# Kernel optimization log

Hardware: AMD Instinct MI355X
Metric: run time of the kernel (lower is better)

The kernel has to match this reference:

```python
import jax, jax.numpy as jnp
import numpy as np

V = 5023      # CoMA mesh vertices
K = 8         # avg neighbors per vertex
E = V * K     # edges
B = 64        # batch
C_IN = 3      # xyz
C_HID = 64    # conv width (layer_info)
M = 9         # kernel_size: number of weight matrices
LATENT = 128


def fsc_conv(x, src, dst, aw, u, c, W, b):
    """Feature-steered graph conv (translation invariant: v = -u).
    x: [B,V,C]; edge e: (i=src[e], j=dst[e]) with adjacency weight aw[e].
    y_i = b + sum_j a_ij * sum_m softmax_m(u_m.(x_i-x_j)+c_m) * (x_j @ W_m)
    """
    Bx, Vx, C = x.shape
    D = W.shape[2]
    xi = x[:, src]                                  # [B,E,C]
    xj = x[:, dst]                                  # [B,E,C]
    logits = jnp.einsum('bec,cm->bem', xi - xj, u) + c   # [B,E,M]
    att = jax.nn.softmax(logits, axis=-1) * aw[None, :, None]
    y = jnp.zeros((Bx, Vx, D), x.dtype)
    for m in range(W.shape[0]):                     # small fixed loop over M
        agg = jnp.zeros((Bx, Vx, C), x.dtype).at[:, src].add(att[:, :, m:m + 1] * xj)
        y = y + agg @ W[m]
    return y + b


def setup_inputs() -> dict:
    key = jax.random.key(0)
    ks = jax.random.split(key, 16)
    x = jax.random.normal(ks[0], (B, V, C_IN), jnp.float32)
    # mesh-like adjacency: each vertex i has K random neighbors, weight 1/K
    src = jnp.repeat(jnp.arange(V, dtype=jnp.int32), K)
    dst = jax.random.randint(ks[1], (E,), 0, V, dtype=jnp.int32)
    aw = jnp.full((E,), 1.0 / K, jnp.float32)
    g = lambda k, shp, fan: jax.random.normal(k, shp, jnp.float32) * np.float32(np.sqrt(2.0 / fan))
    # encoder conv params
    u_e = g(ks[2], (C_IN, M), C_IN + M)
    c_e = jnp.zeros((M,), jnp.float32)
    W_e = g(ks[3], (M, C_IN, C_HID), C_IN + C_HID)
    b_e = jnp.zeros((C_HID,), jnp.float32)
    # encoder latent dense: [V*C_HID, LATENT]
    W_enc = g(ks[4], (V * C_HID, LATENT), V * C_HID)
    b_enc = jnp.zeros((LATENT,), jnp.float32)
    # decoder latent dense: [LATENT, C_HID*V]
    W_dec = g(ks[5], (LATENT, C_HID * V), LATENT)
    b_dec = jnp.zeros((C_HID * V,), jnp.float32)
    # decoder conv params
    u_d = g(ks[6], (C_HID, M), C_HID + M)
    c_d = jnp.zeros((M,), jnp.float32)
    W_d = g(ks[7], (M, C_HID, C_IN), C_HID + C_IN)
    b_d = jnp.zeros((C_IN,), jnp.float32)
    return {'x': x, 'aw': aw, 'u_e': u_e, 'c_e': c_e, 'W_e': W_e, 'b_e': b_e,
            'W_enc': W_enc, 'b_enc': b_enc, 'W_dec': W_dec, 'b_dec': b_dec,
            'u_d': u_d, 'c_d': c_d, 'W_d': W_d, 'b_d': b_d,
            'src': src, 'dst': dst}


def reference(x, aw, u_e, c_e, W_e, b_e, W_enc, b_enc, W_dec, b_dec,
              u_d, c_d, W_d, b_d, src, dst):
    # Encoder: feature-steered conv -> relu -> flatten -> dense to latent
    h = jax.nn.relu(fsc_conv(x, src, dst, aw, u_e, c_e, W_e, b_e))   # [B,V,C_HID]
    z = h.reshape(h.shape[0], -1) @ W_enc + b_enc                    # [B,LATENT]
    # Decoder: dense -> reshape [B,V,C_HID] -> feature-steered conv -> relu
    d = (z @ W_dec + b_dec).reshape(z.shape[0], V, -1)               # [B,V,C_HID]
    out = jax.nn.relu(fsc_conv(d, src, dst, aw, u_d, c_d, W_d, b_d)) # [B,V,3]
    return out
```

## Files before the change

### kernel.cpp

```cpp
#include <hip/hip_runtime.h>

#define VN 5023
#define KN 8
#define BN 64
#define CIN 3
#define CH 64
#define MN 9
#define LAT 128
#define KTOT (VN*CH)
#define NBV (BN*VN)
#define KC 256
#define NCHUNK 1256
#define RED_G 8
#define RED_J 157
#define NXCD 8

__global__ __launch_bounds__(256, 4) void k_conv1(
    const float* __restrict__ x, const float* __restrict__ aw,
    const int* __restrict__ dst,
    const float* __restrict__ u_e, const float* __restrict__ c_e,
    const float* __restrict__ W_e, const float* __restrict__ b_e,
    float* __restrict__ h)
{
  int t = blockIdx.x*256 + threadIdx.x;
  if (t >= NBV) return;
  int b = t / VN, v = t - b*VN;
  const float* xb = x + (size_t)b*VN*CIN;
  float xi0 = xb[v*3+0], xi1 = xb[v*3+1], xi2 = xb[v*3+2];
  float Ti[MN];
#pragma unroll
  for (int m=0;m<MN;m++)
    Ti[m] = xi0*u_e[m] + xi1*u_e[MN+m] + xi2*u_e[2*MN+m] + c_e[m];
  float agg[27];
#pragma unroll
  for (int i=0;i<27;i++) agg[i]=0.f;
  for (int k=0;k<KN;k++){
    int e = v*KN+k;
    int j = dst[e];
    float awe = aw[e];
    float xj0 = xb[j*3+0], xj1 = xb[j*3+1], xj2 = xb[j*3+2];
    float lg[MN];
#pragma unroll
    for (int m=0;m<MN;m++)
      lg[m] = Ti[m] - (xj0*u_e[m]+xj1*u_e[MN+m]+xj2*u_e[2*MN+m]);
    float mx = lg[0];
#pragma unroll
    for (int m=1;m<MN;m++) mx = fmaxf(mx, lg[m]);
    float ex[MN], s=0.f;
#pragma unroll
    for (int m=0;m<MN;m++){ ex[m] = __expf(lg[m]-mx); s += ex[m]; }
    float r = awe / s;
#pragma unroll
    for (int m=0;m<MN;m++){
      float a = ex[m]*r;
      agg[m*3+0] += a*xj0; agg[m*3+1] += a*xj1; agg[m*3+2] += a*xj2;
    }
  }
  float* hr = h + (size_t)t*CH;
  for (int cc=0; cc<4; cc++){
    float y[16];
#pragma unroll
    for (int c=0;c<16;c++) y[c] = b_e[cc*16+c];
#pragma unroll
    for (int mc=0; mc<27; mc++){
      float a = agg[mc];
#pragma unroll
      for (int c=0;c<16;c++) y[c] += a * W_e[mc*CH + cc*16 + c];
    }
#pragma unroll
    for (int c=0;c<16;c+=4){
      float4 o = make_float4(fmaxf(y[c],0.f),fmaxf(y[c+1],0.f),
                             fmaxf(y[c+2],0.f),fmaxf(y[c+3],0.f));
      *(float4*)(hr + cc*16 + c) = o;
    }
  }
}

__global__ __launch_bounds__(256, 4) void k_enc(
    const float* __restrict__ h, const float* __restrict__ We,
    float* __restrict__ partial)
{
  __shared__ float wlds[2][32*128];
  __shared__ float hlds[2][32][68];
  int t = threadIdx.x;
  int blk = blockIdx.x;
  int lq = t & 15;
  int bq = t >> 4;
  float acc[8][4];
#pragma unroll
  for (int i=0;i<8;i++)
#pragma unroll
    for (int j=0;j<4;j++) acc[i][j]=0.f;
  int kbase0 = blk*KC;
  int ldb = t & 63;
  int seg = t >> 6;
  int nt0 = (blk == NCHUNK-1) ? 6 : 8;

  float4 wreg0, wreg1, wreg2, wreg3, hreg0, hreg1;
  {
    const float* wsrc = We + (size_t)kbase0*LAT;
    wreg0 = *(const float4*)(wsrc + 0*1024 + t*4);
    wreg1 = *(const float4*)(wsrc + 1*1024 + t*4);
    wreg2 = *(const float4*)(wsrc + 2*1024 + t*4);
    wreg3 = *(const float4*)(wsrc + 3*1024 + t*4);
    const float* hsrc = h + (size_t)ldb*KTOT + kbase0 + seg*8;
    hreg0 = *(const float4*)(hsrc);
    hreg1 = *(const float4*)(hsrc + 4);
    *(float4*)(&wlds[0][0*1024 + t*4]) = wreg0;
    *(float4*)(&wlds[0][1*1024 + t*4]) = wreg1;
    *(float4*)(&wlds[0][2*1024 + t*4]) = wreg2;
    *(float4*)(&wlds[0][3*1024 + t*4]) = wreg3;
    hlds[0][seg*8+0][ldb]=hreg0.x; hlds[0][seg*8+1][ldb]=hreg0.y;
    hlds[0][seg*8+2][ldb]=hreg0.z; hlds[0][seg*8+3][ldb]=hreg0.w;
    hlds[0][seg*8+4][ldb]=hreg1.x; hlds[0][seg*8+5][ldb]=hreg1.y;
    hlds[0][seg*8+6][ldb]=hreg1.z; hlds[0][seg*8+7][ldb]=hreg1.w;
  }
  __syncthreads();

  int cur = 0;
  for (int t0=0; t0<nt0; t0++){
    bool pf = (t0+1 < nt0);
    if (pf){
      int kbase = kbase0 + (t0+1)*32;
      const float* wsrc = We + (size_t)kbase*LAT;
      wreg0 = *(const float4*)(wsrc + 0*1024 + t*4);
      wreg1 = *(const float4*)(wsrc + 1*1024 + t*4);
      wreg2 = *(const float4*)(wsrc + 2*1024 + t*4);
      wreg3 = *(const float4*)(wsrc + 3*1024 + t*4);
      const float* hsrc = h + (size_t)ldb*KTOT + kbase + seg*8;
      hreg0 = *(const float4*)(hsrc);
      hreg1 = *(const float4*)(hsrc + 4);
    }
    __builtin_amdgcn_sched_barrier(0);
#pragma unroll 4
    for (int kk=0; kk<32; kk++){
      const float* wr = &wlds[cur][kk*128 + lq*8];
      float4 w0 = *(const float4*)wr;
      float4 w1 = *(const float4*)(wr+4);
      float4 z  = *(const float4*)(&hlds[cur][kk][bq*4]);
      float wv[8] = {w0.x,w0.y,w0.z,w0.w,w1.x,w1.y,w1.z,w1.w};
      float zv[4] = {z.x,z.y,z.z,z.w};
#pragma unroll
      for (int li=0;li<8;li++)
#pragma unroll
        for (int bi=0;bi<4;bi++) acc[li][bi] += wv[li]*zv[bi];
    }
    if (pf){
      int nb = cur^1;
      *(float4*)(&wlds[nb][0*1024 + t*4]) = wreg0;
      *(float4*)(&wlds[nb][1*1024 + t*4]) = wreg1;
      *(float4*)(&wlds[nb][2*1024 + t*4]) = wreg2;
      *(float4*)(&wlds[nb][3*1024 + t*4]) = wreg3;
      hlds[nb][seg*8+0][ldb]=hreg0.x; hlds[nb][seg*8+1][ldb]=hreg0.y;
      hlds[nb][seg*8+2][ldb]=hreg0.z; hlds[nb][seg*8+3][ldb]=hreg0.w;
      hlds[nb][seg*8+4][ldb]=hreg1.x; hlds[nb][seg*8+5][ldb]=hreg1.y;
      hlds[nb][seg*8+6][ldb]=hreg1.z; hlds[nb][seg*8+7][ldb]=hreg1.w;
    }
    __syncthreads();
    cur ^= 1;
  }
  float* pp = partial + (size_t)blk*(BN*LAT);
#pragma unroll
  for (int bi=0;bi<4;bi++){
    int b = bq*4+bi;
    float4 o0 = make_float4(acc[0][bi],acc[1][bi],acc[2][bi],acc[3][bi]);
    float4 o1 = make_float4(acc[4][bi],acc[5][bi],acc[6][bi],acc[7][bi]);
    *(float4*)(pp + b*LAT + lq*8)   = o0;
    *(float4*)(pp + b*LAT + lq*8+4) = o1;
  }
}

__global__ __launch_bounds__(256) void k_red1(
    const float* __restrict__ partial, float* __restrict__ partial2)
{
  int idx = blockIdx.x*256 + threadIdx.x;
  int g = blockIdx.y;
  float s = 0.f;
  for (int j=0;j<RED_J;j++)
    s += partial[(size_t)(g + RED_G*j)*(BN*LAT) + idx];
  partial2[(size_t)g*(BN*LAT) + idx] = s;
}

__global__ __launch_bounds__(256) void k_red2(
    const float* __restrict__ partial2, const float* __restrict__ b_enc,
    float* __restrict__ zT)
{
  int idx = blockIdx.x*256 + threadIdx.x;
  float s = 0.f;
#pragma unroll
  for (int g=0; g<RED_G; g++) s += partial2[(size_t)g*(BN*LAT) + idx];
  int b = idx >> 7, l = idx & 127;
  zT[l*BN + b] = s + b_enc[l];
}

__global__ __launch_bounds__(512, 4) void k_dec(
    const float* __restrict__ zT, const float* __restrict__ Wd,
    const float* __restrict__ b_dec, float* __restrict__ d)
{
  int t = threadIdx.x;
  int lane = t & 63;
  int wv = __builtin_amdgcn_readfirstlane(t >> 6);
  int vc = blockIdx.x*256 + lane*4;
  int vs = vc < (KTOT-4) ? vc : (KTOT-4);
  const float* wp = Wd + vs;
  const float* zrow = zT + wv*8;
  float acc[4][8];
#pragma unroll
  for (int i=0;i<4;i++)
#pragma unroll
    for (int j=0;j<8;j++) acc[i][j]=0.f;

  float4 wA[4], wB[4];
#pragma unroll
  for (int u=0;u<4;u++) wA[u] = *(const float4*)(wp + (size_t)u*KTOT);

  for (int l0=0; l0<LAT; l0+=8){
#pragma unroll
    for (int u=0;u<4;u++) wB[u] = *(const float4*)(wp + (size_t)(l0+4+u)*KTOT);
    __builtin_amdgcn_sched_barrier(0);
#pragma unroll
    for (int u=0;u<4;u++){
      int l = l0+u;
      float zv[8];
#pragma unroll
      for (int j=0;j<8;j++) zv[j] = zrow[l*BN + j];
      float wvv[4] = {wA[u].x,wA[u].y,wA[u].z,wA[u].w};
#pragma unroll
      for (int i=0;i<4;i++)
#pragma unroll
        for (int j=0;j<8;j++) acc[i][j] += wvv[i]*zv[j];
    }
    if (l0+8 < LAT){
#pragma unroll
      for (int u=0;u<4;u++) wA[u] = *(const float4*)(wp + (size_t)(l0+8+u)*KTOT);
    }
    __builtin_amdgcn_sched_barrier(0);
#pragma unroll
    for (int u=0;u<4;u++){
      int l = l0+4+u;
      float zv[8];
#pragma unroll
      for (int j=0;j<8;j++) zv[j] = zrow[l*BN + j];
      float wvv[4] = {wB[u].x,wB[u].y,wB[u].z,wB[u].w};
#pragma unroll
      for (int i=0;i<4;i++)
#pragma unroll
        for (int j=0;j<8;j++) acc[i][j] += wvv[i]*zv[j];
    }
  }
  if (vc < KTOT){
    float4 bd = *(const float4*)(b_dec + vc);
#pragma unroll
    for (int j=0;j<8;j++){
      int b = wv*8 + j;
      float4 o = make_float4(acc[0][j]+bd.x, acc[1][j]+bd.y,
                             acc[2][j]+bd.z, acc[3][j]+bd.w);
      *(float4*)(d + (size_t)b*KTOT + vc) = o;
    }
  }
}

__global__ __launch_bounds__(256, 4) void k_tg(
    const float* __restrict__ d, const float* __restrict__ u_d,
    const float* __restrict__ W_d, float* __restrict__ TG)
{
  int t = blockIdx.x*256 + threadIdx.x;
  if (t >= NBV) return;
  const float* drow = d + (size_t)t*CH;
  float T[MN], G[27];
#pragma unroll
  for (int m=0;m<MN;m++) T[m]=0.f;
#pragma unroll
  for (int i=0;i<27;i++) G[i]=0.f;
  for (int c0=0;c0<CH;c0+=4){
    float4 dv = *(const float4*)(drow+c0);
    float dvv[4] = {dv.x,dv.y,dv.z,dv.w};
#pragma unroll
    for (int j=0;j<4;j++){
      int c = c0+j;
      float xv = dvv[j];
#pragma unroll
      for (int m=0;m<MN;m++) T[m] += xv*u_d[c*MN+m];
#pragma unroll
      for (int m=0;m<MN;m++){
        G[m*3+0] += xv*W_d[(m*CH+c)*3+0];
        G[m*3+1] += xv*W_d[(m*CH+c)*3+1];
        G[m*3+2] += xv*W_d[(m*CH+c)*3+2];
      }
    }
  }
  float* tg = TG + (size_t)t*36;
  float rr[36] = {T[0],T[1],T[2],T[3],T[4],T[5],T[6],T[7],T[8],
                  G[0],G[1],G[2],G[3],G[4],G[5],G[6],G[7],G[8],
                  G[9],G[10],G[11],G[12],G[13],G[14],G[15],G[16],G[17],
                  G[18],G[19],G[20],G[21],G[22],G[23],G[24],G[25],G[26]};
#pragma unroll
  for (int i=0;i<36;i+=4)
    *(float4*)(tg+i) = make_float4(rr[i],rr[i+1],rr[i+2],rr[i+3]);
}

__global__ __launch_bounds__(256, 4) void k_att(
    const float* __restrict__ TG, const float* __restrict__ aw,
    const int* __restrict__ dst, const float* __restrict__ c_d,
    const float* __restrict__ b_d, float* __restrict__ out)
{
  int wg = blockIdx.x;
  int wgid = (wg & 7)*157 + (wg >> 3);
  int t = wgid*256 + threadIdx.x;
  if (t >= NBV) return;
  int b = t / VN, v = t - b*VN;
  const float* TGb = TG + (size_t)b*VN*36;
  int e0 = v*KN;
  int4 j01 = *(const int4*)(dst + e0);
  int4 j23 = *(const int4*)(dst + e0 + 4);
  int jj[8] = {j01.x,j01.y,j01.z,j01.w, j23.x,j23.y,j23.z,j23.w};
  float4 a01 = *(const float4*)(aw + e0);
  float4 a23 = *(const float4*)(aw + e0 + 4);
  float awv[8] = {a01.x,a01.y,a01.z,a01.w, a23.x,a23.y,a23.z,a23.w};
  float Ti[MN];
#pragma unroll
  for (int m=0;m<MN;m++) Ti[m] = TGb[(size_t)v*36+m] + c_d[m];
  float y0=0.f, y1=0.f, y2=0.f;
  float4 q[9];
  {
    const float* Rp = TGb + (size_t)jj[0]*36;
#pragma unroll
    for (int i=0;i<9;i++) q[i] = *(const float4*)(Rp + i*4);
  }
#pragma unroll
  for (int k=0;k<KN;k++){
    float4 p[9];
    if (k+1 < KN){
      const float* Rp = TGb + (size_t)jj[k+1]*36;
#pragma unroll
      for (int i=0;i<9;i++) p[i] = *(const float4*)(Rp + i*4);
    }
    float rr[36] = {q[0].x,q[0].y,q[0].z,q[0].w, q[1].x,q[1].y,q[1].z,q[1].w,
                    q[2].x,q[2].y,q[2].z,q[2].w, q[3].x,q[3].y,q[3].z,q[3].w,
                    q[4].x,q[4].y,q[4].z,q[4].w, q[5].x,q[5].y,q[5].z,q[5].w,
                    q[6].x,q[6].y,q[6].z,q[6].w, q[7].x,q[7].y,q[7].z,q[7].w,
                    q[8].x,q[8].y,q[8].z,q[8].w};
    float lg[MN];
#pragma unroll
    for (int m=0;m<MN;m++) lg[m] = Ti[m] - rr[m];
    float mx = lg[0];
#pragma unroll
    for (int m=1;m<MN;m++) mx = fmaxf(mx, lg[m]);
    float ex[MN], s=0.f;
#pragma unroll
    for (int m=0;m<MN;m++){ ex[m] = __expf(lg[m]-mx); s += ex[m]; }
    float sc = awv[k] / s;
#pragma unroll
    for (int m=0;m<MN;m++){
      float a = ex[m]*sc;
      y0 += a*rr[9+m*3+0]; y1 += a*rr[9+m*3+1]; y2 += a*rr[9+m*3+2];
    }
    if (k+1 < KN){
#pragma unroll
      for (int i=0;i<9;i++) q[i] = p[i];
    }
  }
  float* o = out + (size_t)t*3;
  o[0]=fmaxf(y0+b_d[0],0.f); o[1]=fmaxf(y1+b_d[1],0.f); o[2]=fmaxf(y2+b_d[2],0.f);
}

extern "C" void kernel_launch(void* const* d_in, const int* in_sizes, int n_in,
                              void* d_out, int out_size, void* d_ws, size_t ws_size,
                              hipStream_t stream) {
  const float* x     = (const float*)d_in[0];
  const float* aw    = (const float*)d_in[1];
  const float* u_e   = (const float*)d_in[2];
  const float* c_e   = (const float*)d_in[3];
  const float* W_e   = (const float*)d_in[4];
  const float* b_e   = (const float*)d_in[5];
  const float* W_enc = (const float*)d_in[6];
  const float* b_enc = (const float*)d_in[7];
  const float* W_dec = (const float*)d_in[8];
  const float* b_dec = (const float*)d_in[9];
  const float* u_d   = (const float*)d_in[10];
  const float* c_d   = (const float*)d_in[11];
  const float* W_d   = (const float*)d_in[12];
  const float* b_d   = (const float*)d_in[13];
  const int*   dst   = (const int*)d_in[15];
  float* out = (float*)d_out;

  char* ws = (char*)d_ws;
  float* hbuf = (float*)ws;
  size_t off1 = (size_t)NBV*CH*sizeof(float);
  float* partial = (float*)(ws + off1);
  float* TGbuf   = (float*)(ws + off1);
  size_t offz = off1 + (size_t)NCHUNK*(BN*LAT)*sizeof(float);
  float* zT       = (float*)(ws + offz);
  float* partial2 = (float*)(ws + offz + (size_t)(BN*LAT)*sizeof(float));

  int grid_bv = (NBV + 255)/256;

  k_conv1<<<grid_bv,256,0,stream>>>(x, aw, dst, u_e, c_e, W_e, b_e, hbuf);
  k_enc<<<NCHUNK,256,0,stream>>>(hbuf, W_enc, partial);
  dim3 gr1(32, RED_G);
  k_red1<<<gr1,256,0,stream>>>(partial, partial2);
  k_red2<<<32,256,0,stream>>>(partial2, b_enc, zT);
  int grid_dec = (KTOT + 255)/256;
  k_dec<<<grid_dec,512,0,stream>>>(zT, W_dec, b_dec, hbuf);
  k_tg<<<grid_bv,256,0,stream>>>(hbuf, u_d, W_d, TGbuf);
  k_att<<<grid_bv,256,0,stream>>>(TGbuf, aw, dst, c_d, b_d, out);
}
```

Baseline: 347.6 us.

## Use direct global-to-LDS loads in encoder GEMM, larger K chunks, batched conv1 gathers

```diff
diff --git a/kernel.cpp b/kernel.cpp
--- a/kernel.cpp
+++ b/kernel.cpp
@@ -9,9 +9,9 @@
 #define LAT 128
 #define KTOT (VN*CH)
 #define NBV (BN*VN)
-#define KC 256
-#define NCHUNK 1256
-#define RED_G 8
+#define KC 512
+#define NCHUNK 628
+#define RED_G 4
 #define RED_J 157
 #define NXCD 8
 
@@ -26,6 +26,20 @@
   if (t >= NBV) return;
   int b = t / VN, v = t - b*VN;
   const float* xb = x + (size_t)b*VN*CIN;
+  int e0 = v*KN;
+  int4 j01 = *(const int4*)(dst + e0);
+  int4 j23 = *(const int4*)(dst + e0 + 4);
+  int jj[8] = {j01.x,j01.y,j01.z,j01.w, j23.x,j23.y,j23.z,j23.w};
+  float4 a01 = *(const float4*)(aw + e0);
+  float4 a23 = *(const float4*)(aw + e0 + 4);
+  float awv[8] = {a01.x,a01.y,a01.z,a01.w, a23.x,a23.y,a23.z,a23.w};
+  float xj0[8], xj1[8], xj2[8];
+#pragma unroll
+  for (int k=0;k<KN;k++){
+    const float* xr = xb + (size_t)jj[k]*3;
+    xj0[k]=xr[0]; xj1[k]=xr[1]; xj2[k]=xr[2];
+  }
+  __builtin_amdgcn_sched_barrier(0);
   float xi0 = xb[v*3+0], xi1 = xb[v*3+1], xi2 = xb[v*3+2];
   float Ti[MN];
 #pragma unroll
@@ -34,26 +48,23 @@
   float agg[27];
 #pragma unroll
   for (int i=0;i<27;i++) agg[i]=0.f;
+#pragma unroll
   for (int k=0;k<KN;k++){
-    int e = v*KN+k;
-    int j = dst[e];
-    float awe = aw[e];
-    float xj0 = xb[j*3+0], xj1 = xb[j*3+1], xj2 = xb[j*3+2];
     float lg[MN];
 #pragma unroll
     for (int m=0;m<MN;m++)
-      lg[m] = Ti[m] - (xj0*u_e[m]+xj1*u_e[MN+m]+xj2*u_e[2*MN+m]);
+      lg[m] = Ti[m] - (xj0[k]*u_e[m]+xj1[k]*u_e[MN+m]+xj2[k]*u_e[2*MN+m]);
     float mx = lg[0];
 #pragma unroll
     for (int m=1;m<MN;m++) mx = fmaxf(mx, lg[m]);
     float ex[MN], s=0.f;
 #pragma unroll
     for (int m=0;m<MN;m++){ ex[m] = __expf(lg[m]-mx); s += ex[m]; }
-    float r = awe / s;
+    float r = awv[k] / s;
 #pragma unroll
     for (int m=0;m<MN;m++){
       float a = ex[m]*r;
-      agg[m*3+0] += a*xj0; agg[m*3+1] += a*xj1; agg[m*3+2] += a*xj2;
+      agg[m*3+0] += a*xj0[k]; agg[m*3+1] += a*xj1[k]; agg[m*3+2] += a*xj2[k];
     }
   }
   float* hr = h + (size_t)t*CH;
@@ -94,22 +105,19 @@
   int kbase0 = blk*KC;
   int ldb = t & 63;
   int seg = t >> 6;
-  int nt0 = (blk == NCHUNK-1) ? 6 : 8;
-
-  float4 wreg0, wreg1, wreg2, wreg3, hreg0, hreg1;
+  int nt0 = (blk == NCHUNK-1) ? 14 : 16;
+
   {
     const float* wsrc = We + (size_t)kbase0*LAT;
-    wreg0 = *(const float4*)(wsrc + 0*1024 + t*4);
-    wreg1 = *(const float4*)(wsrc + 1*1024 + t*4);
-    wreg2 = *(const float4*)(wsrc + 2*1024 + t*4);
-    wreg3 = *(const float4*)(wsrc + 3*1024 + t*4);
+#pragma unroll
+    for (int q=0;q<4;q++)
+      __builtin_amdgcn_global_load_lds(
+        (const __attribute__((address_space(1))) void*)(wsrc + (q*256+t)*4),
+        (__attribute__((address_space(3))) void*)(&wlds[0][(q*256+t)*4]),
+        16, 0, 0);
     const float* hsrc = h + (size_t)ldb*KTOT + kbase0 + seg*8;
-    hreg0 = *(const float4*)(hsrc);
-    hreg1 = *(const float4*)(hsrc + 4);
-    *(float4*)(&wlds[0][0*1024 + t*4]) = wreg0;
-    *(float4*)(&wlds[0][1*1024 + t*4]) = wreg1;
-    *(float4*)(&wlds[0][2*1024 + t*4]) = wreg2;
-    *(float4*)(&wlds[0][3*1024 + t*4]) = wreg3;
+    float4 hreg0 = *(const float4*)(hsrc);
+    float4 hreg1 = *(const float4*)(hsrc + 4);
     hlds[0][seg*8+0][ldb]=hreg0.x; hlds[0][seg*8+1][ldb]=hreg0.y;
     hlds[0][seg*8+2][ldb]=hreg0.z; hlds[0][seg*8+3][ldb]=hreg0.w;
     hlds[0][seg*8+4][ldb]=hreg1.x; hlds[0][seg*8+5][ldb]=hreg1.y;
@@ -120,13 +128,17 @@
   int cur = 0;
   for (int t0=0; t0<nt0; t0++){
     bool pf = (t0+1 < nt0);
+    float4 hreg0, hreg1;
     if (pf){
       int kbase = kbase0 + (t0+1)*32;
+      int nb = cur^1;
       const float* wsrc = We + (size_t)kbase*LAT;
-      wreg0 = *(const float4*)(wsrc + 0*1024 + t*4);
-      wreg1 = *(const float4*)(wsrc + 1*1024 + t*4);
-      wreg2 = *(const float4*)(wsrc + 2*1024 + t*4);
-      wreg3 = *(const float4*)(wsrc + 3*1024 + t*4);
+#pragma unroll
+      for (int q=0;q<4;q++)
+        __builtin_amdgcn_global_load_lds(
+          (const __attribute__((address_space(1))) void*)(wsrc + (q*256+t)*4),
+          (__attribute__((address_space(3))) void*)(&wlds[nb][(q*256+t)*4]),
+          16, 0, 0);
       const float* hsrc = h + (size_t)ldb*KTOT + kbase + seg*8;
       hreg0 = *(const float4*)(hsrc);
       hreg1 = *(const float4*)(hsrc + 4);
@@ -147,10 +159,6 @@
     }
     if (pf){
       int nb = cur^1;
-      *(float4*)(&wlds[nb][0*1024 + t*4]) = wreg0;
-      *(float4*)(&wlds[nb][1*1024 + t*4]) = wreg1;
-      *(float4*)(&wlds[nb][2*1024 + t*4]) = wreg2;
-      *(float4*)(&wlds[nb][3*1024 + t*4]) = wreg3;
       hlds[nb][seg*8+0][ldb]=hreg0.x; hlds[nb][seg*8+1][ldb]=hreg0.y;
       hlds[nb][seg*8+2][ldb]=hreg0.z; hlds[nb][seg*8+3][ldb]=hreg0.w;
       hlds[nb][seg*8+4][ldb]=hreg1.x; hlds[nb][seg*8+5][ldb]=hreg1.y;
@@ -389,7 +397,7 @@
   size_t off1 = (size_t)NBV*CH*sizeof(float);
   float* partial = (float*)(ws + off1);
   float* TGbuf   = (float*)(ws + off1);
-  size_t offz = off1 + (size_t)NCHUNK*(BN*LAT)*sizeof(float);
+  size_t offz = off1 + (size_t)NCHUNK*(BN*LAT)*sizeof(float) + 4096;
   float* zT       = (float*)(ws + offz);
   float* partial2 = (float*)(ws + offz + (size_t)(BN*LAT)*sizeof(float));
 
```

Result: slower. 355.7 us (+2.4%).
